# Kernel tuning notes

Measured on AMD Instinct MI355X. Metric: run time of the kernel, lower is better.

## Reference

```python
import jax, jax.numpy as jnp
import numpy as np

N = 100000
E = 1600000
D_IN = 128
D_H = 256


def setup_inputs() -> dict:
    key = jax.random.key(0)
    ks = jax.random.split(key, 8)
    x = jax.random.normal(ks[0], (N, D_IN), dtype=jnp.float32)
    x_tilde = jax.random.normal(ks[1], (N, D_IN), dtype=jnp.float32)
    adj_row = jnp.sort(jax.random.randint(ks[2], (E,), 0, N, dtype=jnp.int32))
    adj_col = jax.random.randint(ks[3], (E,), 0, N, dtype=jnp.int32)
    # normalized-ish positive edge weights
    adj_vals = jax.random.uniform(ks[4], (E,), dtype=jnp.float32) / 16.0
    # Linear weight (torch layout [out, in]), xavier-ish scale
    W1 = jax.random.normal(ks[5], (D_H, D_IN), dtype=jnp.float32) * (2.0 / (D_IN + D_H)) ** 0.5
    prelu_a = jnp.full((1,), 0.25, dtype=jnp.float32)  # PReLU default slope
    w_bil = jax.random.normal(ks[6], (D_H, D_H), dtype=jnp.float32) * (2.0 / (2 * D_H)) ** 0.5
    return {"x": x, "x_tilde": x_tilde, "adj_vals": adj_vals, "adj_row": adj_row,
            "adj_col": adj_col, "W1": W1, "prelu_a": prelu_a, "w_bil": w_bil}


def reference(x, x_tilde, adj_vals, adj_row, adj_col, W1, prelu_a, w_bil):
    n = x.shape[0]

    def gcn(feat):
        # SpMM: agg[r] = sum_e vals[e] * feat[col[e]] for edges with row[e]==r
        gathered = adj_vals[:, None] * feat[adj_col]  # [E, D_IN]
        agg = jax.ops.segment_sum(gathered, adj_row, num_segments=n)  # [N, D_IN]
        z = agg @ W1.T  # [N, D_H]
        return jnp.where(z >= 0, z, prelu_a[0] * z)  # PReLU

    h = gcn(x)
    h_tilde = gcn(x_tilde)
    s = jax.nn.sigmoid(jnp.mean(h, axis=0))  # [D_H] readout (same for every row)
    dp = jnp.einsum('ni,ij,j->n', h, w_bil, s)  # bilinear discriminator
    dn = jnp.einsum('ni,ij,j->n', h_tilde, w_bil, s)
    return jnp.concatenate([dp, dn])[None, :]  # [1, 2N]
```

## Files before the change

kernel.cpp:

```cpp
#include <hip/hip_runtime.h>


__device__ __forceinline__ float b2f(unsigned short s) {
    union { unsigned int u; float f; } c; c.u = ((unsigned int)s) << 16; return c.f;
}
__device__ __forceinline__ unsigned short f2b(float f) {
    union { float f; unsigned int u; } c; c.f = f;
    unsigned int u = c.u;
    unsigned int r = u + 0x7FFFu + ((u >> 16) & 1u);
    return (unsigned short)(r >> 16);
}
__device__ __forceinline__ unsigned int pack2(float lo, float hi) {
    return ((unsigned int)f2b(hi) << 16) | f2b(lo);
}
__device__ __forceinline__ void fma8(float* a, float v, uint4 w) {
    a[0] = fmaf(v, b2f((unsigned short)w.x), a[0]);
    a[1] = fmaf(v, b2f((unsigned short)(w.x >> 16)), a[1]);
    a[2] = fmaf(v, b2f((unsigned short)w.y), a[2]);
    a[3] = fmaf(v, b2f((unsigned short)(w.y >> 16)), a[3]);
    a[4] = fmaf(v, b2f((unsigned short)w.z), a[4]);
    a[5] = fmaf(v, b2f((unsigned short)(w.z >> 16)), a[5]);
    a[6] = fmaf(v, b2f((unsigned short)w.w), a[6]);
    a[7] = fmaf(v, b2f((unsigned short)(w.w >> 16)), a[7]);
}

typedef __attribute__((ext_vector_type(8))) short bf16x8;
typedef __attribute__((ext_vector_type(4))) float f32x4;

#define T_TILES 10

__global__ __launch_bounds__(256) void prep(
    const int* __restrict__ row, int* __restrict__ rp, int n, int e, int rb,
    const float* __restrict__ w1, unsigned short* __restrict__ w1b, int pb,
    const float* __restrict__ x, const float* __restrict__ xt,
    unsigned short* __restrict__ xint, int total8, int halfcb)
{
    int b = blockIdx.x, tid = threadIdx.x;
    if (b < rb) {
        int i = b * 256 + tid;
        if (i > e) return;
        if (i == 0) {
            int r1 = row[0];
            for (int rr = 0; rr <= r1; ++rr) rp[rr] = 0;
        } else if (i == e) {
            int r0 = row[e - 1];
            for (int rr = r0 + 1; rr <= n; ++rr) rp[rr] = e;
        } else {
            int r0 = row[i - 1], r1 = row[i];
            for (int rr = r0 + 1; rr <= r1; ++rr) rp[rr] = i;
        }
    } else if (b < rb + pb) {
        int i = (b - rb) * 256 + tid;
        if (i < 32768) w1b[i] = f2b(w1[i]);
    } else {
        int cb = b - rb - pb;
        int which = (cb >= halfcb) ? 1 : 0;
        int i = (cb - which * halfcb) * 256 + tid;
        if (i >= total8) return;
        const float* s = which ? xt : x;
        int node = i >> 4, sub = i & 15;
        const float4* p = (const float4*)s + (size_t)i * 2;
        float4 a = p[0], bb = p[1];
        uint4 o;
        o.x = pack2(a.x, a.y);  o.y = pack2(a.z, a.w);
        o.z = pack2(bb.x, bb.y); o.w = pack2(bb.z, bb.w);
        *(uint4*)(xint + (size_t)node * 256 + which * 128 + sub * 8) = o;
    }
}

__global__ __launch_bounds__(256) void spmm_dual4(
    const unsigned short* __restrict__ xint, const float* __restrict__ vals,
    const int* __restrict__ col, const int* __restrict__ row_ptr,
    unsigned short* __restrict__ aggx, unsigned short* __restrict__ aggt, int n)
{
    int wave = threadIdx.x >> 6;
    int lane = threadIdx.x & 63;
    int g = lane >> 4, l = lane & 15;
    int r = blockIdx.x * 4 + wave;
    if (r >= n) return;
    int e0 = row_ptr[r], e1 = row_ptr[r + 1];
    float ax[8], at[8];
#pragma unroll
    for (int d = 0; d < 8; ++d) { ax[d] = 0.f; at[d] = 0.f; }
    for (int chunk = e0; chunk < e1; chunk += 64) {
        int m = e1 - chunk; if (m > 64) m = 64;
        int ce = chunk + (lane < m ? lane : m - 1);
        int cc = col[ce];
        float cv = (lane < m) ? vals[ce] : 0.f;
        for (int base = 0; base < m; base += 16) {
            uint4 xw[4], tw[4];
            float fv[4];
#pragma unroll
            for (int u = 0; u < 4; ++u) {
                int idx = base + 4 * u + g;
                int idc = idx < m ? idx : m - 1;
                int c  = __shfl(cc, idc, 64);
                float v = __shfl(cv, idc, 64);
                fv[u] = (idx < m) ? v : 0.f;
                const uint4* p = (const uint4*)(xint + (size_t)c * 256);
                xw[u] = p[l];
                tw[u] = p[16 + l];
            }
#pragma unroll
            for (int u = 0; u < 4; ++u) { fma8(ax, fv[u], xw[u]); fma8(at, fv[u], tw[u]); }
        }
    }
#pragma unroll
    for (int d = 0; d < 8; ++d) {
        ax[d] += __shfl_xor(ax[d], 16, 64);
        ax[d] += __shfl_xor(ax[d], 32, 64);
        at[d] += __shfl_xor(at[d], 16, 64);
        at[d] += __shfl_xor(at[d], 32, 64);
    }
    if (g == 0) {
        uint4 o;
        o.x = pack2(ax[0], ax[1]); o.y = pack2(ax[2], ax[3]);
        o.z = pack2(ax[4], ax[5]); o.w = pack2(ax[6], ax[7]);
        ((uint4*)(aggx + (size_t)r * 128))[l] = o;
    } else if (g == 1) {
        uint4 o;
        o.x = pack2(at[0], at[1]); o.y = pack2(at[2], at[3]);
        o.z = pack2(at[4], at[5]); o.w = pack2(at[6], at[7]);
        ((uint4*)(aggt + (size_t)r * 128))[l] = o;
    }
}

__global__ __launch_bounds__(256) void gemm_colsum3(
    const short* __restrict__ aggb, const short* __restrict__ w1,
    const float* __restrict__ pa, float* __restrict__ partial, int ntiles, int nb)
{
    int tid = threadIdx.x;
    int w = tid >> 6, lane = tid & 63;
    int nl = lane & 15, quad = lane >> 4;
    const short* brow = w1 + ((size_t)(4 * w) * 16 + nl) * 128 + quad * 8;
    bf16x8 bf[4][4];
#pragma unroll
    for (int j = 0; j < 4; ++j)
#pragma unroll
        for (int k = 0; k < 4; ++k)
            bf[j][k] = *(const bf16x8*)(brow + j * 2048 + k * 32);
    float aslope = pa[0];
    float cs[4] = {0.f, 0.f, 0.f, 0.f};
    int t0 = blockIdx.x * T_TILES;
    int nt = ntiles - t0; if (nt > T_TILES) nt = T_TILES;
    for (int i = 0; i < nt; ++i) {
        const short* arow = aggb + ((size_t)(t0 + i) * 16 + nl) * 128 + quad * 8;
        bf16x8 af[4];
#pragma unroll
        for (int k = 0; k < 4; ++k) af[k] = *(const bf16x8*)(arow + k * 32);
        f32x4 acc[4];
#pragma unroll
        for (int j = 0; j < 4; ++j) acc[j] = (f32x4){0.f, 0.f, 0.f, 0.f};
#pragma unroll
        for (int k = 0; k < 4; ++k)
#pragma unroll
            for (int j = 0; j < 4; ++j)
                acc[j] = __builtin_amdgcn_mfma_f32_16x16x32_bf16(af[k], bf[j][k], acc[j], 0, 0, 0);
#pragma unroll
        for (int j = 0; j < 4; ++j)
#pragma unroll
            for (int r = 0; r < 4; ++r) {
                float z = acc[j][r];
                cs[j] += (z >= 0.f) ? z : aslope * z;
            }
    }
#pragma unroll
    for (int j = 0; j < 4; ++j) {
        cs[j] += __shfl_xor(cs[j], 16, 64);
        cs[j] += __shfl_xor(cs[j], 32, 64);
    }
    if (quad == 0)
#pragma unroll
        for (int j = 0; j < 4; ++j)
            partial[(size_t)((4 * w + j) * 16 + nl) * nb + blockIdx.x] = cs[j];
}

__global__ __launch_bounds__(256) void reduce_sig(
    const float* __restrict__ partial, int nb, float* __restrict__ s_out, float invN)
{
    __shared__ float l[256];
    int d = blockIdx.x, tid = threadIdx.x;
    float s = 0.f;
    for (int i = tid; i < nb; i += 256)
        s += partial[(size_t)d * nb + i];
    l[tid] = s;
    __syncthreads();
    for (int o = 128; o > 0; o >>= 1) {
        if (tid < o) l[tid] += l[tid + o];
        __syncthreads();
    }
    if (tid == 0) s_out[d] = 1.f / (1.f + expf(-l[0] * invN));
}

__global__ __launch_bounds__(256) void compute_v(
    const float* __restrict__ s_in, const float* __restrict__ wbil,
    float* __restrict__ v)
{
    __shared__ float s_lds[256];
    int t = threadIdx.x;
    s_lds[t] = s_in[t];
    __syncthreads();
    const float* wrow = wbil + (size_t)t * 256;
    float acc = 0.f;
#pragma unroll 8
    for (int j = 0; j < 256; ++j)
        acc = fmaf(wrow[j], s_lds[j], acc);
    v[t] = acc;
}

__global__ __launch_bounds__(256) void gemm_dp2(
    const short* __restrict__ aggx, const short* __restrict__ aggt,
    const short* __restrict__ w1, const float* __restrict__ pa,
    const float* __restrict__ v, float* __restrict__ out, int ntiles, int N)
{
    __shared__ float dpbuf[4][T_TILES * 16];
    int tid = threadIdx.x;
    int w = tid >> 6, lane = tid & 63;
    int nl = lane & 15, quad = lane >> 4;
    const short* agg = blockIdx.y ? aggt : aggx;
    const short* brow = w1 + ((size_t)(4 * w) * 16 + nl) * 128 + quad * 8;
    bf16x8 bf[4][4];
#pragma unroll
    for (int j = 0; j < 4; ++j)
#pragma unroll
        for (int k = 0; k < 4; ++k)
            bf[j][k] = *(const bf16x8*)(brow + j * 2048 + k * 32);
    float vreg[4];
#pragma unroll
    for (int j = 0; j < 4; ++j) vreg[j] = v[(4 * w + j) * 16 + nl];
    float aslope = pa[0];
    int t0 = blockIdx.x * T_TILES;
    int nt = ntiles - t0; if (nt > T_TILES) nt = T_TILES;
    for (int i = 0; i < nt; ++i) {
        const short* arow = agg + ((size_t)(t0 + i) * 16 + nl) * 128 + quad * 8;
        bf16x8 af[4];
#pragma unroll
        for (int k = 0; k < 4; ++k) af[k] = *(const bf16x8*)(arow + k * 32);
        f32x4 acc[4];
#pragma unroll
        for (int j = 0; j < 4; ++j) acc[j] = (f32x4){0.f, 0.f, 0.f, 0.f};
#pragma unroll
        for (int k = 0; k < 4; ++k)
#pragma unroll
            for (int j = 0; j < 4; ++j)
                acc[j] = __builtin_amdgcn_mfma_f32_16x16x32_bf16(af[k], bf[j][k], acc[j], 0, 0, 0);
        float p[4] = {0.f, 0.f, 0.f, 0.f};
#pragma unroll
        for (int j = 0; j < 4; ++j)
#pragma unroll
            for (int r = 0; r < 4; ++r) {
                float z = acc[j][r];
                float h = (z >= 0.f) ? z : aslope * z;
                p[r] = fmaf(h, vreg[j], p[r]);
            }
#pragma unroll
        for (int r = 0; r < 4; ++r) {
            p[r] += __shfl_xor(p[r], 1, 64);
            p[r] += __shfl_xor(p[r], 2, 64);
            p[r] += __shfl_xor(p[r], 4, 64);
            p[r] += __shfl_xor(p[r], 8, 64);
        }
        if (nl == 0)
#pragma unroll
            for (int r = 0; r < 4; ++r)
                dpbuf[w][i * 16 + quad * 4 + r] = p[r];
    }
    __syncthreads();
    int nloc = nt * 16;
    for (int idx = tid; idx < nloc; idx += 256) {
        float s = dpbuf[0][idx] + dpbuf[1][idx] + dpbuf[2][idx] + dpbuf[3][idx];
        out[(size_t)blockIdx.y * N + (size_t)t0 * 16 + idx] = s;
    }
}

extern "C" void kernel_launch(void* const* d_in, const int* in_sizes, int n_in,
                              void* d_out, int out_size, void* d_ws, size_t ws_size,
                              hipStream_t stream) {
    const float* x    = (const float*)d_in[0];
    const float* xt   = (const float*)d_in[1];
    const float* vals = (const float*)d_in[2];
    const int* row    = (const int*)d_in[3];
    const int* col    = (const int*)d_in[4];
    const float* w1   = (const float*)d_in[5];
    const float* pa   = (const float*)d_in[6];
    const float* wb   = (const float*)d_in[7];

    const int N = in_sizes[0] / 128;
    const int E = in_sizes[2];
    const int ntiles = (N + 15) / 16;
    const int cs_blocks = (ntiles + T_TILES - 1) / T_TILES;

    char* ws = (char*)d_ws;
    size_t off = 0;
    auto alloc = [&](size_t bytes) { char* p = ws + off; off = (off + bytes + 255) & ~(size_t)255; return p; };
    int* row_ptr         = (int*)alloc((size_t)(N + 1) * 4);
    unsigned short* aggx = (unsigned short*)alloc((size_t)N * 128 * 2);
    unsigned short* aggt = (unsigned short*)alloc((size_t)N * 128 * 2);
    unsigned short* w1b  = (unsigned short*)alloc(32768 * 2);
    float* partial       = (float*)alloc((size_t)cs_blocks * 256 * 4);
    float* svec          = (float*)alloc(256 * 4);
    float* vvec          = (float*)alloc(256 * 4);
    unsigned short* xint = (unsigned short*)alloc((size_t)N * 256 * 2);

    int rb = (E + 1 + 255) / 256;
    int pb = 128;
    int total8 = (N * 128) / 8;
    int halfcb = (total8 + 255) / 256;
    prep<<<rb + pb + 2 * halfcb, 256, 0, stream>>>(
        row, row_ptr, N, E, rb, w1, w1b, pb, x, xt, xint, total8, halfcb);

    spmm_dual4<<<(N + 3) / 4, 256, 0, stream>>>(xint, vals, col, row_ptr, aggx, aggt, N);

    gemm_colsum3<<<cs_blocks, 256, 0, stream>>>(
        (const short*)aggx, (const short*)w1b, pa, partial, ntiles, cs_blocks);
    reduce_sig<<<256, 256, 0, stream>>>(partial, cs_blocks, svec, 1.0f / (float)N);
    compute_v<<<1, 256, 0, stream>>>(svec, wb, vvec);
    gemm_dp2<<<dim3(cs_blocks, 2), 256, 0, stream>>>(
        (const short*)aggx, (const short*)aggt, (const short*)w1b, pa, vvec,
        (float*)d_out, ntiles, N);
}
```

Measured before the change: 337.2 us.

## Map one row per 16-lane group in SpMM and parallelize bilinear vector

The SpMM kernel now gives each 16-lane quarter-wave its own row (16 rows per block) instead of one row per wave split across four edge groups. This removes the cross-group shuffle reduction and the idle lanes on short rows, at the cost of more divergence when row lengths differ within a wave. compute_v becomes 256 single-wave blocks that reduce with shuffles, replacing one block that ran serial 256-length dot products. T_TILES drops from 10 to 5, which changes per-block tiling in the GEMM kernels.

Measured after the change: 342.3 us. About the same (+1.5%).

```diff
diff --git a/kernel.cpp b/kernel.cpp
--- a/kernel.cpp
+++ b/kernel.cpp
@@ -27,7 +27,7 @@
 typedef __attribute__((ext_vector_type(8))) short bf16x8;
 typedef __attribute__((ext_vector_type(4))) float f32x4;
 
-#define T_TILES 10
+#define T_TILES 5
 
 __global__ __launch_bounds__(256) void prep(
     const int* __restrict__ row, int* __restrict__ rp, int n, int e, int rb,
@@ -68,7 +68,7 @@
     }
 }
 
-__global__ __launch_bounds__(256) void spmm_dual4(
+__global__ __launch_bounds__(256) void spmm_group(
     const unsigned short* __restrict__ xint, const float* __restrict__ vals,
     const int* __restrict__ col, const int* __restrict__ row_ptr,
     unsigned short* __restrict__ aggx, unsigned short* __restrict__ aggt, int n)
@@ -76,52 +76,46 @@
     int wave = threadIdx.x >> 6;
     int lane = threadIdx.x & 63;
     int g = lane >> 4, l = lane & 15;
-    int r = blockIdx.x * 4 + wave;
-    if (r >= n) return;
-    int e0 = row_ptr[r], e1 = row_ptr[r + 1];
+    int r = blockIdx.x * 16 + wave * 4 + g;
+    bool valid = (r < n);
+    int rc = valid ? r : (n - 1);
+    int e0 = row_ptr[rc], e1 = row_ptr[rc + 1];
+    if (!valid) e1 = e0;
     float ax[8], at[8];
 #pragma unroll
     for (int d = 0; d < 8; ++d) { ax[d] = 0.f; at[d] = 0.f; }
-    for (int chunk = e0; chunk < e1; chunk += 64) {
-        int m = e1 - chunk; if (m > 64) m = 64;
-        int ce = chunk + (lane < m ? lane : m - 1);
+    for (int base = e0; base < e1; base += 16) {
+        int m = e1 - base; if (m > 16) m = 16;
+        int ce = base + (l < m ? l : m - 1);
         int cc = col[ce];
-        float cv = (lane < m) ? vals[ce] : 0.f;
-        for (int base = 0; base < m; base += 16) {
+        float cv = (l < m) ? vals[ce] : 0.f;
+        for (int k = 0; k < m; k += 4) {
             uint4 xw[4], tw[4];
             float fv[4];
 #pragma unroll
-            for (int u = 0; u < 4; ++u) {
-                int idx = base + 4 * u + g;
+            for (int j = 0; j < 4; ++j) {
+                int idx = k + j;
                 int idc = idx < m ? idx : m - 1;
-                int c  = __shfl(cc, idc, 64);
-                float v = __shfl(cv, idc, 64);
-                fv[u] = (idx < m) ? v : 0.f;
+                int c  = __shfl(cc, g * 16 + idc, 64);
+                float v = __shfl(cv, g * 16 + idc, 64);
+                fv[j] = (idx < m) ? v : 0.f;
                 const uint4* p = (const uint4*)(xint + (size_t)c * 256);
-                xw[u] = p[l];
-                tw[u] = p[16 + l];
+                xw[j] = p[l];
+                tw[j] = p[16 + l];
             }
 #pragma unroll
-            for (int u = 0; u < 4; ++u) { fma8(ax, fv[u], xw[u]); fma8(at, fv[u], tw[u]); }
+            for (int j = 0; j < 4; ++j) { fma8(ax, fv[j], xw[j]); fma8(at, fv[j], tw[j]); }
         }
     }
-#pragma unroll
-    for (int d = 0; d < 8; ++d) {
-        ax[d] += __shfl_xor(ax[d], 16, 64);
-        ax[d] += __shfl_xor(ax[d], 32, 64);
-        at[d] += __shfl_xor(at[d], 16, 64);
-        at[d] += __shfl_xor(at[d], 32, 64);
-    }
-    if (g == 0) {
+    if (valid) {
         uint4 o;
         o.x = pack2(ax[0], ax[1]); o.y = pack2(ax[2], ax[3]);
         o.z = pack2(ax[4], ax[5]); o.w = pack2(ax[6], ax[7]);
         ((uint4*)(aggx + (size_t)r * 128))[l] = o;
-    } else if (g == 1) {
-        uint4 o;
-        o.x = pack2(at[0], at[1]); o.y = pack2(at[2], at[3]);
-        o.z = pack2(at[4], at[5]); o.w = pack2(at[6], at[7]);
-        ((uint4*)(aggt + (size_t)r * 128))[l] = o;
+        uint4 q;
+        q.x = pack2(at[0], at[1]); q.y = pack2(at[2], at[3]);
+        q.z = pack2(at[4], at[5]); q.w = pack2(at[6], at[7]);
+        ((uint4*)(aggt + (size_t)r * 128))[l] = q;
     }
 }
 
@@ -192,20 +186,24 @@
     if (tid == 0) s_out[d] = 1.f / (1.f + expf(-l[0] * invN));
 }
 
-__global__ __launch_bounds__(256) void compute_v(
+__global__ __launch_bounds__(64) void compute_v2(
     const float* __restrict__ s_in, const float* __restrict__ wbil,
     float* __restrict__ v)
 {
-    __shared__ float s_lds[256];
-    int t = threadIdx.x;
-    s_lds[t] = s_in[t];
-    __syncthreads();
-    const float* wrow = wbil + (size_t)t * 256;
+    int d = blockIdx.x;
+    int lane = threadIdx.x;
+    const float* wrow = wbil + (size_t)d * 256;
     float acc = 0.f;
-#pragma unroll 8
-    for (int j = 0; j < 256; ++j)
-        acc = fmaf(wrow[j], s_lds[j], acc);
-    v[t] = acc;
+#pragma unroll
+    for (int j = 0; j < 4; ++j)
+        acc = fmaf(wrow[j * 64 + lane], s_in[j * 64 + lane], acc);
+    acc += __shfl_xor(acc, 1, 64);
+    acc += __shfl_xor(acc, 2, 64);
+    acc += __shfl_xor(acc, 4, 64);
+    acc += __shfl_xor(acc, 8, 64);
+    acc += __shfl_xor(acc, 16, 64);
+    acc += __shfl_xor(acc, 32, 64);
+    if (lane == 0) v[d] = acc;
 }
 
 __global__ __launch_bounds__(256) void gemm_dp2(
@@ -309,12 +307,12 @@
     prep<<<rb + pb + 2 * halfcb, 256, 0, stream>>>(
         row, row_ptr, N, E, rb, w1, w1b, pb, x, xt, xint, total8, halfcb);
 
-    spmm_dual4<<<(N + 3) / 4, 256, 0, stream>>>(xint, vals, col, row_ptr, aggx, aggt, N);
+    spmm_group<<<(N + 15) / 16, 256, 0, stream>>>(xint, vals, col, row_ptr, aggx, aggt, N);
 
     gemm_colsum3<<<cs_blocks, 256, 0, stream>>>(
         (const short*)aggx, (const short*)w1b, pa, partial, ntiles, cs_blocks);
     reduce_sig<<<256, 256, 0, stream>>>(partial, cs_blocks, svec, 1.0f / (float)N);
-    compute_v<<<1, 256, 0, stream>>>(svec, wb, vvec);
+    compute_v2<<<256, 64, 0, stream>>>(svec, wb, vvec);
     gemm_dp2<<<dim3(cs_blocks, 2), 256, 0, stream>>>(
         (const short*)aggx, (const short*)aggt, (const short*)w1b, pa, vvec,
         (float*)d_out, ntiles, N);
```

## Make SpMM persistent with rows-per-wave, parallelize compute_v, halve GEMM tile count

Applied to the files above, without the earlier changes.

Replaces the one-wave-per-row SpMM launch with a fixed grid of 2048 blocks where each wave handles a contiguous run of rows. The wave loads the run's row_ptr slice once and shares it with shuffles. compute_v moves from one 256-thread block doing serial dot products to 256 single-wave blocks that reduce with shuffles. T_TILES drops from 10 to 5, which changes the tiles per block in the GEMM kernels and likely the block count. The persistent layout cuts launch and scheduling overhead, but rows within a wave run one after another, which may reduce memory-level parallelism and worsen load balance when row degrees vary.

Measured after the change: 343.7 us. Within noise of the previous version (+1.9%).

```diff
diff --git a/kernel.cpp b/kernel.cpp
--- a/kernel.cpp
+++ b/kernel.cpp
@@ -27,7 +27,7 @@
 typedef __attribute__((ext_vector_type(8))) short bf16x8;
 typedef __attribute__((ext_vector_type(4))) float f32x4;
 
-#define T_TILES 10
+#define T_TILES 5
 
 __global__ __launch_bounds__(256) void prep(
     const int* __restrict__ row, int* __restrict__ rp, int n, int e, int rb,
@@ -68,60 +68,68 @@
     }
 }
 
-__global__ __launch_bounds__(256) void spmm_dual4(
+__global__ __launch_bounds__(256) void spmm_persist(
     const unsigned short* __restrict__ xint, const float* __restrict__ vals,
     const int* __restrict__ col, const int* __restrict__ row_ptr,
-    unsigned short* __restrict__ aggx, unsigned short* __restrict__ aggt, int n)
-{
-    int wave = threadIdx.x >> 6;
+    unsigned short* __restrict__ aggx, unsigned short* __restrict__ aggt,
+    int n, int rpw)
+{
+    int wid = blockIdx.x * 4 + (threadIdx.x >> 6);
     int lane = threadIdx.x & 63;
     int g = lane >> 4, l = lane & 15;
-    int r = blockIdx.x * 4 + wave;
-    if (r >= n) return;
-    int e0 = row_ptr[r], e1 = row_ptr[r + 1];
-    float ax[8], at[8];
-#pragma unroll
-    for (int d = 0; d < 8; ++d) { ax[d] = 0.f; at[d] = 0.f; }
-    for (int chunk = e0; chunk < e1; chunk += 64) {
-        int m = e1 - chunk; if (m > 64) m = 64;
-        int ce = chunk + (lane < m ? lane : m - 1);
-        int cc = col[ce];
-        float cv = (lane < m) ? vals[ce] : 0.f;
-        for (int base = 0; base < m; base += 16) {
-            uint4 xw[4], tw[4];
-            float fv[4];
-#pragma unroll
-            for (int u = 0; u < 4; ++u) {
-                int idx = base + 4 * u + g;
-                int idc = idx < m ? idx : m - 1;
-                int c  = __shfl(cc, idc, 64);
-                float v = __shfl(cv, idc, 64);
-                fv[u] = (idx < m) ? v : 0.f;
-                const uint4* p = (const uint4*)(xint + (size_t)c * 256);
-                xw[u] = p[l];
-                tw[u] = p[16 + l];
+    int r0 = wid * rpw;
+    if (r0 >= n) return;
+    int rend = r0 + rpw; if (rend > n) rend = n;
+    int rpslice = row_ptr[(r0 + lane <= n) ? (r0 + lane) : n];
+
+    for (int r = r0; r < rend; ++r) {
+        int i = r - r0;
+        int e0 = __shfl(rpslice, i, 64);
+        int e1 = __shfl(rpslice, i + 1, 64);
+        float ax[8], at[8];
+#pragma unroll
+        for (int d = 0; d < 8; ++d) { ax[d] = 0.f; at[d] = 0.f; }
+        for (int chunk = e0; chunk < e1; chunk += 64) {
+            int m = e1 - chunk; if (m > 64) m = 64;
+            int ce = chunk + (lane < m ? lane : m - 1);
+            int cc = col[ce];
+            float cv = (lane < m) ? vals[ce] : 0.f;
+            for (int base = 0; base < m; base += 16) {
+                uint4 xw[4], tw[4];
+                float fv[4];
+#pragma unroll
+                for (int u = 0; u < 4; ++u) {
+                    int idx = base + 4 * u + g;
+                    int idc = idx < m ? idx : m - 1;
+                    int c  = __shfl(cc, idc, 64);
+                    float v = __shfl(cv, idc, 64);
+                    fv[u] = (idx < m) ? v : 0.f;
+                    const uint4* p = (const uint4*)(xint + (size_t)c * 256);
+                    xw[u] = p[l];
+                    tw[u] = p[16 + l];
+                }
+#pragma unroll
+                for (int u = 0; u < 4; ++u) { fma8(ax, fv[u], xw[u]); fma8(at, fv[u], tw[u]); }
             }
-#pragma unroll
-            for (int u = 0; u < 4; ++u) { fma8(ax, fv[u], xw[u]); fma8(at, fv[u], tw[u]); }
-        }
-    }
-#pragma unroll
-    for (int d = 0; d < 8; ++d) {
-        ax[d] += __shfl_xor(ax[d], 16, 64);
-        ax[d] += __shfl_xor(ax[d], 32, 64);
-        at[d] += __shfl_xor(at[d], 16, 64);
-        at[d] += __shfl_xor(at[d], 32, 64);
-    }
-    if (g == 0) {
-        uint4 o;
-        o.x = pack2(ax[0], ax[1]); o.y = pack2(ax[2], ax[3]);
-        o.z = pack2(ax[4], ax[5]); o.w = pack2(ax[6], ax[7]);
-        ((uint4*)(aggx + (size_t)r * 128))[l] = o;
-    } else if (g == 1) {
-        uint4 o;
-        o.x = pack2(at[0], at[1]); o.y = pack2(at[2], at[3]);
-        o.z = pack2(at[4], at[5]); o.w = pack2(at[6], at[7]);
-        ((uint4*)(aggt + (size_t)r * 128))[l] = o;
+        }
+#pragma unroll
+        for (int d = 0; d < 8; ++d) {
+            ax[d] += __shfl_xor(ax[d], 16, 64);
+            ax[d] += __shfl_xor(ax[d], 32, 64);
+            at[d] += __shfl_xor(at[d], 16, 64);
+            at[d] += __shfl_xor(at[d], 32, 64);
+        }
+        if (g == 0) {
+            uint4 o;
+            o.x = pack2(ax[0], ax[1]); o.y = pack2(ax[2], ax[3]);
+            o.z = pack2(ax[4], ax[5]); o.w = pack2(ax[6], ax[7]);
+            ((uint4*)(aggx + (size_t)r * 128))[l] = o;
+        } else if (g == 1) {
+            uint4 o;
+            o.x = pack2(at[0], at[1]); o.y = pack2(at[2], at[3]);
+            o.z = pack2(at[4], at[5]); o.w = pack2(at[6], at[7]);
+            ((uint4*)(aggt + (size_t)r * 128))[l] = o;
+        }
     }
 }
 
@@ -192,20 +200,24 @@
     if (tid == 0) s_out[d] = 1.f / (1.f + expf(-l[0] * invN));
 }
 
-__global__ __launch_bounds__(256) void compute_v(
+__global__ __launch_bounds__(64) void compute_v2(
     const float* __restrict__ s_in, const float* __restrict__ wbil,
     float* __restrict__ v)
 {
-    __shared__ float s_lds[256];
-    int t = threadIdx.x;
-    s_lds[t] = s_in[t];
-    __syncthreads();
-    const float* wrow = wbil + (size_t)t * 256;
+    int d = blockIdx.x;
+    int lane = threadIdx.x;
+    const float* wrow = wbil + (size_t)d * 256;
     float acc = 0.f;
-#pragma unroll 8
-    for (int j = 0; j < 256; ++j)
-        acc = fmaf(wrow[j], s_lds[j], acc);
-    v[t] = acc;
+#pragma unroll
+    for (int j = 0; j < 4; ++j)
+        acc = fmaf(wrow[j * 64 + lane], s_in[j * 64 + lane], acc);
+    acc += __shfl_xor(acc, 1, 64);
+    acc += __shfl_xor(acc, 2, 64);
+    acc += __shfl_xor(acc, 4, 64);
+    acc += __shfl_xor(acc, 8, 64);
+    acc += __shfl_xor(acc, 16, 64);
+    acc += __shfl_xor(acc, 32, 64);
+    if (lane == 0) v[d] = acc;
 }
 
 __global__ __launch_bounds__(256) void gemm_dp2(
@@ -309,12 +321,16 @@
     prep<<<rb + pb + 2 * halfcb, 256, 0, stream>>>(
         row, row_ptr, N, E, rb, w1, w1b, pb, x, xt, xint, total8, halfcb);
 
-    spmm_dual4<<<(N + 3) / 4, 256, 0, stream>>>(xint, vals, col, row_ptr, aggx, aggt, N);
+    int spmm_blocks = 2048;
+    int nwaves = spmm_blocks * 4;
+    int rpw = (N + nwaves - 1) / nwaves;
+    spmm_persist<<<spmm_blocks, 256, 0, stream>>>(
+        xint, vals, col, row_ptr, aggx, aggt, N, rpw);
 
     gemm_colsum3<<<cs_blocks, 256, 0, stream>>>(
         (const short*)aggx, (const short*)w1b, pa, partial, ntiles, cs_blocks);
     reduce_sig<<<256, 256, 0, stream>>>(partial, cs_blocks, svec, 1.0f / (float)N);
-    compute_v<<<1, 256, 0, stream>>>(svec, wb, vvec);
+    compute_v2<<<256, 64, 0, stream>>>(svec, wb, vvec);
     gemm_dp2<<<dim3(cs_blocks, 2), 256, 0, stream>>>(
         (const short*)aggx, (const short*)aggt, (const short*)w1b, pa, vvec,
         (float*)d_out, ntiles, N);
```

## Fuse column-sum reduction, sigmoid and bilinear vector into GEMM via last-block atomics

Applied to the files above, without the earlier changes.

Replaces the per-block partial buffer plus separate reduce_sig and compute_v kernels with atomicAdd into a 256-entry accumulator. A completion counter picks the last block, which applies the sigmoid and computes v = w_bil·s with wave shuffles. The accumulator and counter are zeroed by an extra block in the prep kernel. T_TILES is halved to spread the GEMM over more blocks. This removes two kernel launches and the partial-buffer traffic, but adds atomic contention on 256 addresses and makes the summation order nondeterministic.

After: 464.4 us. 37.7% more time.

```diff
diff --git a/kernel.cpp b/kernel.cpp
--- a/kernel.cpp
+++ b/kernel.cpp
@@ -27,15 +27,21 @@
 typedef __attribute__((ext_vector_type(8))) short bf16x8;
 typedef __attribute__((ext_vector_type(4))) float f32x4;
 
-#define T_TILES 10
+#define T_TILES 5
 
 __global__ __launch_bounds__(256) void prep(
     const int* __restrict__ row, int* __restrict__ rp, int n, int e, int rb,
     const float* __restrict__ w1, unsigned short* __restrict__ w1b, int pb,
     const float* __restrict__ x, const float* __restrict__ xt,
-    unsigned short* __restrict__ xint, int total8, int halfcb)
+    unsigned short* __restrict__ xint, int total8, int halfcb,
+    float* __restrict__ s_accum, unsigned int* __restrict__ done)
 {
     int b = blockIdx.x, tid = threadIdx.x;
+    if (b == rb + pb + 2 * halfcb) {
+        s_accum[tid] = 0.f;
+        if (tid == 0) *done = 0u;
+        return;
+    }
     if (b < rb) {
         int i = b * 256 + tid;
         if (i > e) return;
@@ -125,9 +131,11 @@
     }
 }
 
-__global__ __launch_bounds__(256) void gemm_colsum3(
+__global__ __launch_bounds__(256) void gemm_colsum_fused(
     const short* __restrict__ aggb, const short* __restrict__ w1,
-    const float* __restrict__ pa, float* __restrict__ partial, int ntiles, int nb)
+    const float* __restrict__ pa, float* __restrict__ s_accum,
+    unsigned int* __restrict__ done, const float* __restrict__ wbil,
+    float* __restrict__ vvec, int ntiles, float invN)
 {
     int tid = threadIdx.x;
     int w = tid >> 6, lane = tid & 63;
@@ -172,40 +180,38 @@
     if (quad == 0)
 #pragma unroll
         for (int j = 0; j < 4; ++j)
-            partial[(size_t)((4 * w + j) * 16 + nl) * nb + blockIdx.x] = cs[j];
-}
-
-__global__ __launch_bounds__(256) void reduce_sig(
-    const float* __restrict__ partial, int nb, float* __restrict__ s_out, float invN)
-{
-    __shared__ float l[256];
-    int d = blockIdx.x, tid = threadIdx.x;
-    float s = 0.f;
-    for (int i = tid; i < nb; i += 256)
-        s += partial[(size_t)d * nb + i];
-    l[tid] = s;
+            atomicAdd(&s_accum[(4 * w + j) * 16 + nl], cs[j]);
+
+    __shared__ unsigned int lastflag;
+    __threadfence();
     __syncthreads();
-    for (int o = 128; o > 0; o >>= 1) {
-        if (tid < o) l[tid] += l[tid + o];
+    if (tid == 0) {
+        unsigned int old = atomicAdd(done, 1u);
+        lastflag = (old == gridDim.x - 1) ? 1u : 0u;
+    }
+    __syncthreads();
+    if (lastflag != 0u) {
+        __threadfence();
+        __shared__ float s_lds[256];
+        float sum = atomicAdd(&s_accum[tid], 0.0f);
+        s_lds[tid] = 1.f / (1.f + __expf(-sum * invN));
         __syncthreads();
-    }
-    if (tid == 0) s_out[d] = 1.f / (1.f + expf(-l[0] * invN));
-}
-
-__global__ __launch_bounds__(256) void compute_v(
-    const float* __restrict__ s_in, const float* __restrict__ wbil,
-    float* __restrict__ v)
-{
-    __shared__ float s_lds[256];
-    int t = threadIdx.x;
-    s_lds[t] = s_in[t];
-    __syncthreads();
-    const float* wrow = wbil + (size_t)t * 256;
-    float acc = 0.f;
-#pragma unroll 8
-    for (int j = 0; j < 256; ++j)
-        acc = fmaf(wrow[j], s_lds[j], acc);
-    v[t] = acc;
+        int wv = tid >> 6, ln = tid & 63;
+        for (int d = wv * 64; d < wv * 64 + 64; ++d) {
+            const float* wrow = wbil + (size_t)d * 256;
+            float acc = 0.f;
+#pragma unroll
+            for (int jj = 0; jj < 4; ++jj)
+                acc = fmaf(wrow[jj * 64 + ln], s_lds[jj * 64 + ln], acc);
+            acc += __shfl_xor(acc, 1, 64);
+            acc += __shfl_xor(acc, 2, 64);
+            acc += __shfl_xor(acc, 4, 64);
+            acc += __shfl_xor(acc, 8, 64);
+            acc += __shfl_xor(acc, 16, 64);
+            acc += __shfl_xor(acc, 32, 64);
+            if (ln == 0) vvec[d] = acc;
+        }
+    }
 }
 
 __global__ __launch_bounds__(256) void gemm_dp2(
@@ -297,8 +303,8 @@
     unsigned short* aggx = (unsigned short*)alloc((size_t)N * 128 * 2);
     unsigned short* aggt = (unsigned short*)alloc((size_t)N * 128 * 2);
     unsigned short* w1b  = (unsigned short*)alloc(32768 * 2);
-    float* partial       = (float*)alloc((size_t)cs_blocks * 256 * 4);
-    float* svec          = (float*)alloc(256 * 4);
+    float* s_accum       = (float*)alloc(256 * 4);
+    unsigned int* done   = (unsigned int*)alloc(256);
     float* vvec          = (float*)alloc(256 * 4);
     unsigned short* xint = (unsigned short*)alloc((size_t)N * 256 * 2);
 
@@ -306,15 +312,16 @@
     int pb = 128;
     int total8 = (N * 128) / 8;
     int halfcb = (total8 + 255) / 256;
-    prep<<<rb + pb + 2 * halfcb, 256, 0, stream>>>(
-        row, row_ptr, N, E, rb, w1, w1b, pb, x, xt, xint, total8, halfcb);
+    prep<<<rb + pb + 2 * halfcb + 1, 256, 0, stream>>>(
+        row, row_ptr, N, E, rb, w1, w1b, pb, x, xt, xint, total8, halfcb,
+        s_accum, done);
 
     spmm_dual4<<<(N + 3) / 4, 256, 0, stream>>>(xint, vals, col, row_ptr, aggx, aggt, N);
 
-    gemm_colsum3<<<cs_blocks, 256, 0, stream>>>(
-        (const short*)aggx, (const short*)w1b, pa, partial, ntiles, cs_blocks);
-    reduce_sig<<<256, 256, 0, stream>>>(partial, cs_blocks, svec, 1.0f / (float)N);
-    compute_v<<<1, 256, 0, stream>>>(svec, wb, vvec);
+    gemm_colsum_fused<<<cs_blocks, 256, 0, stream>>>(
+        (const short*)aggx, (const short*)w1b, pa, s_accum, done, wb, vvec,
+        ntiles, 1.0f / (float)N);
+
     gemm_dp2<<<dim3(cs_blocks, 2), 256, 0, stream>>>(
         (const short*)aggx, (const short*)aggt, (const short*)w1b, pa, vvec,
         (float*)d_out, ntiles, N);
```
